# Performance work log

Measured on AMD Instinct MI355X. Metric: run time of the kernel, lower is better.

The kernel has to match this reference:

```python
import jax, jax.numpy as jnp
import numpy as np

NUM_VISUAL = 16
MAX_PATCH = 1024
DIM = 1280
NUM_HEADS = 16
HEAD_DIM = DIM // NUM_HEADS  # 80


def _make_rope_cache(key):
    # cos/sin cache per (visual, patch): (N, P, 1, head_dim*2) = [cos | sin]
    inv_freq = 1.0 / (10000.0 ** (jnp.arange(0, HEAD_DIM, 2, dtype=jnp.float32) / HEAD_DIM))  # (hd/2,)
    pos = jnp.arange(MAX_PATCH, dtype=jnp.float32)  # (P,)
    freqs = pos[:, None] * inv_freq[None, :]              # (P, hd/2)
    emb = jnp.concatenate([freqs, freqs], axis=-1)        # (P, hd)
    cos = jnp.cos(emb)
    sin = jnp.sin(emb)
    cache = jnp.concatenate([cos, sin], axis=-1)          # (P, 2*hd)
    return jnp.broadcast_to(cache[None, :, None, :], (NUM_VISUAL, MAX_PATCH, 1, 2 * HEAD_DIM))


def setup_inputs() -> dict:
    key = jax.random.key(0)
    k1, k2, k3, k4, k5, k6 = jax.random.split(key, 6)
    s = 0.02
    hidden_states = jax.random.normal(k1, (NUM_VISUAL, MAX_PATCH, DIM), dtype=jnp.float32)
    rope_cache = _make_rope_cache(k2)
    seq_lens = jax.random.randint(k3, (NUM_VISUAL,), 512, MAX_PATCH + 1, dtype=jnp.int32)
    w_qkv = jax.random.normal(k4, (3 * DIM, DIM), dtype=jnp.float32) * s
    b_qkv = jnp.zeros((3 * DIM,), dtype=jnp.float32)
    w_proj = jax.random.normal(k5, (DIM, DIM), dtype=jnp.float32) * s
    b_proj = jnp.zeros((DIM,), dtype=jnp.float32)
    return {"hidden_states": hidden_states, "rope_cache": rope_cache, "seq_lens": seq_lens,
            "w_qkv": w_qkv, "b_qkv": b_qkv, "w_proj": w_proj, "b_proj": b_proj}


def _rotate_half(x):
    x1, x2 = jnp.split(x, 2, axis=-1)
    return jnp.concatenate([-x2, x1], axis=-1)


def reference(hidden_states, rope_cache, seq_lens, w_qkv, b_qkv, w_proj, b_proj):
    N, P, D = hidden_states.shape
    H, hd = NUM_HEADS, HEAD_DIM
    # QKV projection: (N, P, 3D) -> (N, P, 3, H, hd)
    qkv = (hidden_states @ w_qkv.T + b_qkv).reshape(N, P, 3, H, hd)
    q, k, v = qkv[:, :, 0], qkv[:, :, 1], qkv[:, :, 2]  # each (N, P, H, hd)
    # RoPE via precomputed cos/sin: rope_cache (N, P, 1, 2*hd)
    cos = rope_cache[..., :hd]   # (N, P, 1, hd), broadcasts over heads
    sin = rope_cache[..., hd:]
    q = q * cos + _rotate_half(q) * sin
    k = k * cos + _rotate_half(k) * sin
    # Attention with key-padding mask (BlockMask equivalent for varlen patches)
    scale = 1.0 / jnp.sqrt(jnp.asarray(hd, dtype=q.dtype))
    scores = jnp.einsum("nqhd,nkhd->nhqk", q, k) * scale  # (N, H, P, P)
    key_valid = jnp.arange(P, dtype=jnp.int32)[None, :] < seq_lens[:, None]  # (N, P)
    neg = jnp.asarray(-1e30, dtype=scores.dtype)
    scores = jnp.where(key_valid[:, None, None, :], scores, neg)
    attn = jax.nn.softmax(scores, axis=-1)
    out = jnp.einsum("nhqk,nkhd->nqhd", attn, v).reshape(N, P, D)
    return out @ w_proj.T + b_proj
```

## Files before the change

### kernel.cpp

```cpp
#include <hip/hip_runtime.h>
#include <stdint.h>

#define DIM     1280
#define NHEADS  16
#define HD      80
#define NV      16
#define MAXP    1024
#define MTOT    (NV*MAXP)

typedef __bf16 bf16;
using bf16x8 = __attribute__((ext_vector_type(8))) __bf16;
using bf16x4 = __attribute__((ext_vector_type(4))) __bf16;
using f32x4  = __attribute__((ext_vector_type(4))) float;

#define GLOAD_LDS16(g, l)                                                     \
    __builtin_amdgcn_global_load_lds(                                         \
        (const __attribute__((address_space(1))) void*)(g),                   \
        (__attribute__((address_space(3))) void*)(l), 16, 0, 0)

__global__ __launch_bounds__(256)
void cvt_bf16(const float* __restrict__ src, bf16* __restrict__ dst, int n4)
{
    const int i = blockIdx.x * 256 + threadIdx.x;
    if (i < n4) {
        const float4 f = ((const float4*)src)[i];
        bf16x4 r;
        r[0] = (bf16)f.x; r[1] = (bf16)f.y; r[2] = (bf16)f.z; r[3] = (bf16)f.w;
        ((bf16x4*)dst)[i] = r;
    }
}

template<bool IS_QKV, int NB, int G>
__global__ __launch_bounds__(256)
void gemm_nt_big(const bf16* __restrict__ A, const bf16* __restrict__ B,
                 const float* __restrict__ bias,
                 bf16* __restrict__ out0, bf16* __restrict__ out1,
                 bf16* __restrict__ out2, float* __restrict__ outf)
{
    const int K = DIM;
    __shared__ __align__(16) bf16 SH[2*128*64];
    bf16* const As = SH;
    bf16* const Bs = SH + 128*64;

    const int tid  = threadIdx.x;
    const int lane = tid & 63, wave = tid >> 6;
    const int quad = lane >> 4, c16 = lane & 15;
    const int wm = wave & 1, wn = wave >> 1;

    const int bid = blockIdx.x;
    const int xcd = bid & 7;
    const int idx = bid >> 3;
    const int nbg = idx / (16*G);
    const int rem = idx % (16*G);
    const int mb  = xcd*16 + rem / G;
    const int nb  = nbg*G  + rem % G;

    const int sr   = lane >> 3;
    const int slot = lane & 7;
    const int sc   = (slot ^ sr) * 8;
    const long a_row0 = (long)mb * 128;
    const long b_row0 = (long)nb * 128;

    const bf16* ga[4];
    const bf16* gb[4];
    #pragma unroll
    for (int c = 0; c < 4; ++c) {
        const int seg = c*4 + wave;
        const int row = seg*8 + sr;
        ga[c] = A + (a_row0 + row)*K + sc;
        gb[c] = B + (b_row0 + row)*K + sc;
    }

    f32x4 acc[4][4] = {};
    const int xr = c16 & 7;

    for (int kt = 0; kt < K/64; ++kt) {
        const int k0 = kt * 64;
        __syncthreads();
        #pragma unroll
        for (int c = 0; c < 4; ++c) {
            const int seg = c*4 + wave;
            GLOAD_LDS16(ga[c] + k0, As + seg*512);
            GLOAD_LDS16(gb[c] + k0, Bs + seg*512);
        }
        __syncthreads();
        #pragma unroll
        for (int kk = 0; kk < 2; ++kk) {
            const int j  = kk*4 + quad;
            const int ko = ((j ^ xr) * 8);
            bf16x8 af[4], bfr[4];
            #pragma unroll
            for (int mt = 0; mt < 4; ++mt)
                af[mt] = *(const bf16x8*)(As + (wm*64 + mt*16 + c16)*64 + ko);
            #pragma unroll
            for (int nt = 0; nt < 4; ++nt)
                bfr[nt] = *(const bf16x8*)(Bs + (wn*64 + nt*16 + c16)*64 + ko);
            #pragma unroll
            for (int mt = 0; mt < 4; ++mt)
                #pragma unroll
                for (int nt = 0; nt < 4; ++nt)
                    acc[mt][nt] = __builtin_amdgcn_mfma_f32_16x16x32_bf16(
                        af[mt], bfr[nt], acc[mt][nt], 0, 0, 0);
        }
    }

    if constexpr (IS_QKV) {
        const int which = nb / 10;
        if (which < 2) {
            bf16* const dst = (which == 0) ? out0 : out1;
            #pragma unroll
            for (int nt = 0; nt < 4; ++nt) {
                const int col = nb*128 + wn*64 + nt*16 + c16;
                const float bv = bias[col];
                const int rr = col - which*DIM;
                const int h  = rr / HD;
                const int d  = rr - h*HD;
                #pragma unroll
                for (int mt = 0; mt < 4; ++mt) {
                    #pragma unroll
                    for (int r = 0; r < 4; ++r) {
                        const int row = mb*128 + wm*64 + mt*16 + quad*4 + r;
                        const int n = row >> 10, p = row & 1023;
                        dst[((long)((n*NHEADS + h)*MAXP + p))*HD + d] =
                            (bf16)(acc[mt][nt][r] + bv);
                    }
                }
            }
        } else {
            __syncthreads();
            #pragma unroll
            for (int nt = 0; nt < 4; ++nt) {
                const int dl0 = wn*64 + nt*16 + c16;
                const float bv = bias[nb*128 + dl0];
                const int swz = (dl0 & 15) << 3;
                #pragma unroll
                for (int mt = 0; mt < 4; ++mt) {
                    #pragma unroll
                    for (int r = 0; r < 4; ++r) {
                        const int pl = wm*64 + mt*16 + quad*4 + r;
                        SH[dl0*128 + (pl ^ swz)] = (bf16)(acc[mt][nt][r] + bv);
                    }
                }
            }
            __syncthreads();
            const int n_    = mb >> 3;
            const int pbase = (mb & 7) * 128;
            #pragma unroll
            for (int it = 0; it < 8; ++it) {
                const int c  = tid + 256*it;
                const int dl = c >> 4, j = c & 15;
                const int p0 = (j ^ (dl & 15)) << 3;
                const int rr = (nb - 20)*128 + dl;
                const int hh = rr / HD;
                const int dd = rr - hh*HD;
                bf16x8 v = *(const bf16x8*)(SH + dl*128 + j*8);
                *(bf16x8*)(out2 + ((long)((n_*NHEADS + hh)*HD + dd))*MAXP
                                  + pbase + p0) = v;
            }
        }
    } else {
        #pragma unroll
        for (int nt = 0; nt < 4; ++nt) {
            const int col = nb*128 + wn*64 + nt*16 + c16;
            const float bv = bias[col];
            #pragma unroll
            for (int mt = 0; mt < 4; ++mt) {
                #pragma unroll
                for (int r = 0; r < 4; ++r) {
                    const int row = mb*128 + wm*64 + mt*16 + quad*4 + r;
                    outf[(long)row*DIM + col] = acc[mt][nt][r] + bv;
                }
            }
        }
    }
}

__global__ __launch_bounds__(320)
void rope_kernel(bf16* __restrict__ qb, bf16* __restrict__ kb,
                 const float* __restrict__ rope)
{
    const int tid = threadIdx.x;
    const int j   = tid % 5;
    const int rl  = tid / 5;
    const long grow = (long)blockIdx.x * 64 + rl;
    const int p = (int)(grow & 1023);
    const int h = (int)((grow >> 10) & 15);
    const int n = (int)((grow >> 14) & 15);
    const int a = (int)(grow >> 18);
    bf16* const arr = a ? kb : qb;
    const long base = ((long)((n*NHEADS + h)*MAXP + p))*HD;
    const float* rc = rope + ((long)(n*MAXP + p))*160;
    const int d = j*8;

    bf16x8 x1v = *(const bf16x8*)(arr + base + d);
    bf16x8 x2v = *(const bf16x8*)(arr + base + 40 + d);

    float c1[8], s1[8], c2[8], s2[8];
    *(float4*)(c1)   = *(const float4*)(rc + d);
    *(float4*)(c1+4) = *(const float4*)(rc + d + 4);
    *(float4*)(s1)   = *(const float4*)(rc + 80 + d);
    *(float4*)(s1+4) = *(const float4*)(rc + 80 + d + 4);
    *(float4*)(c2)   = *(const float4*)(rc + 40 + d);
    *(float4*)(c2+4) = *(const float4*)(rc + 40 + d + 4);
    *(float4*)(s2)   = *(const float4*)(rc + 120 + d);
    *(float4*)(s2+4) = *(const float4*)(rc + 120 + d + 4);

    const float QS = 0.11180339887498949f * 1.4426950408889634f;
    bf16x8 r1, r2;
    #pragma unroll
    for (int i = 0; i < 8; ++i) {
        const float x1 = (float)x1v[i];
        const float x2 = (float)x2v[i];
        float o1 = x1 * c1[i] - x2 * s1[i];
        float o2 = x2 * c2[i] + x1 * s2[i];
        if (a == 0) { o1 *= QS; o2 *= QS; }
        r1[i] = (bf16)o1;
        r2[i] = (bf16)o2;
    }
    *(bf16x8*)(arr + base + d)      = r1;
    *(bf16x8*)(arr + base + 40 + d) = r2;
}

#define ATTN_ISSUE(ktp) do {                                                  \
    const long kro_ = qkbase + (long)(ktp)*64*HD;                             \
    kA = k0v ? *(const float4*)(kb + kro_ + (long)kr0*HD + kc0) : zero4;      \
    kB = k1v ? *(const float4*)(kb + kro_ + (long)kr1*HD + kc1) : zero4;      \
    kC = k2v ? *(const float4*)(kb + kro_ + (long)kr2*HD + kc2) : zero4;      \
    const long vro_ = vbase + (long)(ktp)*64 + vc8;                           \
    vA = *(const float4*)(vt + vro_ + (long)vd0*MAXP);                        \
    vB = *(const float4*)(vt + vro_ + (long)vd1*MAXP);                        \
    if (v2ok) vC = *(const float4*)(vt + vro_ + (long)vd2*MAXP);              \
} while (0)

#define ATTN_COMMIT() do {                                                    \
    *(float4*)(Ks + kr0*104 + kc0) = kA;                                      \
    *(float4*)(Ks + kr1*104 + kc1) = kB;                                      \
    *(float4*)(Ks + kr2*104 + kc2) = kC;                                      \
    *(float4*)(Vts + vd0*72 + vc8) = vA;                                      \
    *(float4*)(Vts + vd1*72 + vc8) = vB;                                      \
    if (v2ok) *(float4*)(Vts + vd2*72 + vc8) = vC;                            \
} while (0)

__global__ __launch_bounds__(256)
void attn_kernel(const bf16* __restrict__ qb, const bf16* __restrict__ kb,
                 const bf16* __restrict__ vt, const int* __restrict__ seq_lens,
                 bf16* __restrict__ outb)
{
    __shared__ __align__(16) bf16 Qs[64*104];
    __shared__ __align__(16) bf16 Ks[64*104];
    __shared__ __align__(16) bf16 Vts[80*72];

    const int tid  = threadIdx.x;
    const int lane = tid & 63, wave = tid >> 6;
    const int quad = lane >> 4, c16 = lane & 15;
    const int qt = blockIdx.x, h = blockIdx.y, n = blockIdx.z;
    const int seqlen = seq_lens[n];

    const long qkbase = ((long)(n*NHEADS + h)) * MAXP * HD;
    const long vbase  = ((long)(n*NHEADS + h)) * HD * MAXP;

    const float4 zero4 = make_float4(0.f, 0.f, 0.f, 0.f);

    const int kr0 = tid / 12,         kc0 = (tid % 12) * 8;
    const int kr1 = (tid + 256) / 12, kc1 = ((tid + 256) % 12) * 8;
    const int kr2 = (tid + 512) / 12, kc2 = ((tid + 512) % 12) * 8;
    const bool k0v = kc0 < 80, k1v = kc1 < 80, k2v = kc2 < 80;
    const int vd0 = tid >> 3, vd1 = vd0 + 32, vd2 = vd0 + 64;
    const int vc8 = (tid & 7) * 8;
    const bool v2ok = tid < 128;

    float4 kA, kB, kC, vA, vB, vC;

    ATTN_ISSUE(0);
    for (int i = tid; i < 768; i += 256) {
        int row = i / 12, c = i % 12;
        float4 v = (c < 10)
            ? *(const float4*)(qb + qkbase + (long)(qt*64 + row)*HD + c*8)
            : zero4;
        *(float4*)(Qs + row*104 + c*8) = v;
    }
    __syncthreads();
    bf16x8 aq[3];
    #pragma unroll
    for (int kc = 0; kc < 3; ++kc)
        aq[kc] = *(const bf16x8*)(Qs + (wave*16 + c16)*104 + kc*32 + quad*8);

    float mrow = -1e30f, lrow = 0.0f;
    f32x4 O[5] = {};

    union U8 { bf16x8 v; bf16x4 h[2]; };

    const int nkt = (seqlen + 63) >> 6;
    for (int kt = 0; kt < nkt; ++kt) {
        __syncthreads();
        ATTN_COMMIT();
        __syncthreads();
        if (kt + 1 < nkt) ATTN_ISSUE(kt + 1);

        f32x4 S[4] = {};
        __builtin_amdgcn_s_setprio(1);
        #pragma unroll
        for (int kc = 0; kc < 3; ++kc) {
            const int ko = kc*32 + quad*8;
            #pragma unroll
            for (int nt = 0; nt < 4; ++nt) {
                bf16x8 ak = *(const bf16x8*)(Ks + (nt*16 + c16)*104 + ko);
                S[nt] = __builtin_amdgcn_mfma_f32_16x16x32_bf16(ak, aq[kc], S[nt], 0,0,0);
            }
        }
        __builtin_amdgcn_s_setprio(0);

        if (kt == nkt - 1) {
            #pragma unroll
            for (int nt = 0; nt < 4; ++nt) {
                const int key0 = kt*64 + nt*16 + quad*4;
                #pragma unroll
                for (int r = 0; r < 4; ++r)
                    if (key0 + r >= seqlen) S[nt][r] = -1e30f;
            }
        }

        float mx[4];
        #pragma unroll
        for (int nt = 0; nt < 4; ++nt)
            mx[nt] = fmaxf(fmaxf(S[nt][0], S[nt][1]), fmaxf(S[nt][2], S[nt][3]));
        float pmax = fmaxf(fmaxf(mx[0], mx[1]), fmaxf(mx[2], mx[3]));
        pmax = fmaxf(pmax, __shfl_xor(pmax, 16));
        pmax = fmaxf(pmax, __shfl_xor(pmax, 32));

        if (!__all(pmax <= mrow + 8.0f)) {
            const float nm    = fmaxf(mrow, pmax);
            const float alpha = exp2f(mrow - nm);
            mrow = nm;
            lrow *= alpha;
            #pragma unroll
            for (int dt = 0; dt < 5; ++dt)
                #pragma unroll
                for (int r = 0; r < 4; ++r)
                    O[dt][r] *= alpha;
        }

        #pragma unroll
        for (int nt = 0; nt < 4; ++nt)
            #pragma unroll
            for (int r = 0; r < 4; ++r)
                S[nt][r] = exp2f(S[nt][r] - mrow);

        float sm[4];
        #pragma unroll
        for (int nt = 0; nt < 4; ++nt)
            sm[nt] = (S[nt][0] + S[nt][1]) + (S[nt][2] + S[nt][3]);
        float rs = (sm[0] + sm[1]) + (sm[2] + sm[3]);
        rs += __shfl_xor(rs, 16);
        rs += __shfl_xor(rs, 32);
        lrow += rs;

        bf16x8 Pk[2];
        #pragma unroll
        for (int nt = 0; nt < 4; ++nt)
            #pragma unroll
            for (int r = 0; r < 4; ++r)
                Pk[nt >> 1][(nt & 1)*4 + r] = (bf16)S[nt][r];

        __builtin_amdgcn_s_setprio(1);
        #pragma unroll
        for (int kc = 0; kc < 2; ++kc) {
            #pragma unroll
            for (int dt = 0; dt < 5; ++dt) {
                U8 av;
                av.h[0] = *(const bf16x4*)(Vts + (dt*16 + c16)*72 + kc*32 + quad*4);
                av.h[1] = *(const bf16x4*)(Vts + (dt*16 + c16)*72 + kc*32 + 16 + quad*4);
                O[dt] = __builtin_amdgcn_mfma_f32_16x16x32_bf16(av.v, Pk[kc], O[dt], 0,0,0);
            }
        }
        __builtin_amdgcn_s_setprio(0);
    }

    const float inv = 1.0f / lrow;
    #pragma unroll
    for (int dt = 0; dt < 5; ++dt)
        #pragma unroll
        for (int r = 0; r < 4; ++r)
            Qs[(wave*16 + c16)*104 + dt*16 + quad*4 + r] = (bf16)(O[dt][r] * inv);
    __syncthreads();
    for (int i = tid; i < 640; i += 256) {
        const int row = i / 10, c = i % 10;
        const float4 v = *(const float4*)(Qs + row*104 + c*8);
        *(float4*)(outb + ((long)(n*MAXP + qt*64 + row))*DIM + h*HD + c*8) = v;
    }
}

extern "C" void kernel_launch(void* const* d_in, const int* in_sizes, int n_in,
                              void* d_out, int out_size, void* d_ws, size_t ws_size,
                              hipStream_t stream)
{
    const float* hidden = (const float*)d_in[0];
    const float* rope   = (const float*)d_in[1];
    const int*   seql   = (const int*)d_in[2];
    const float* wqkv   = (const float*)d_in[3];
    const float* bqkv   = (const float*)d_in[4];
    const float* wproj  = (const float*)d_in[5];
    const float* bproj  = (const float*)d_in[6];
    float* out = (float*)d_out;

    const size_t H_ELEMS  = (size_t)MTOT*DIM;
    const size_t WQ_ELEMS = (size_t)3*DIM*DIM;
    const size_t WP_ELEMS = (size_t)DIM*DIM;
    const size_t QK_ELEMS = (size_t)NV*NHEADS*MAXP*HD;

    bf16* h_bf  = (bf16*)d_ws;
    bf16* wq_bf = h_bf  + H_ELEMS;
    bf16* wp_bf = wq_bf + WQ_ELEMS;

    bf16* q_b = (bf16*)d_out;
    bf16* k_b = q_b + QK_ELEMS;
    bf16* v_t = (bf16*)d_in[0];
    bf16* a_b = v_t + QK_ELEMS;

    cvt_bf16<<<(H_ELEMS/4 + 255)/256, 256, 0, stream>>>(hidden, h_bf, H_ELEMS/4);
    cvt_bf16<<<(WQ_ELEMS/4 + 255)/256, 256, 0, stream>>>(wqkv, wq_bf, WQ_ELEMS/4);
    cvt_bf16<<<(WP_ELEMS/4 + 255)/256, 256, 0, stream>>>(wproj, wp_bf, WP_ELEMS/4);

    gemm_nt_big<true, 30, 6><<<3840, 256, 0, stream>>>(
        h_bf, wq_bf, bqkv, q_b, k_b, v_t, nullptr);

    rope_kernel<<<524288/64, 320, 0, stream>>>(q_b, k_b, rope);

    attn_kernel<<<dim3(MAXP/64, NHEADS, NV), 256, 0, stream>>>(
        q_b, k_b, v_t, seql, a_b);

    gemm_nt_big<false, 10, 10><<<1280, 256, 0, stream>>>(
        a_b, wp_bf, bproj, nullptr, nullptr, nullptr, out);
}
```

Before: 657.2 us.

## Double-buffer GEMM LDS tiles and stage Q/K epilogue through shared memory

The GEMM main loop now uses two LDS buffers, issuing the next k-tile's global-to-LDS loads before computing the current one, with manual vmcnt waits and barriers. The aim is to overlap memory latency with MFMA work. The Q/K epilogue now writes the accumulator into swizzled LDS first and then emits 16-byte vector stores to the head-major output, replacing scattered 2-byte stores. This doubles LDS use to 64KB per block, which may reduce occupancy. The Q/K vector stores also assume 8-column groups never cross an 80-wide head boundary; this holds because 80 is a multiple of 8.

```diff
diff --git a/kernel.cpp b/kernel.cpp
--- a/kernel.cpp
+++ b/kernel.cpp
@@ -30,6 +30,17 @@
     }
 }
 
+#define GEMM_STAGE(dA, dB, koff) do {                                         \
+    GLOAD_LDS16(ga[0] + (koff), (dA) + (0*4 + wave)*512);                     \
+    GLOAD_LDS16(gb[0] + (koff), (dB) + (0*4 + wave)*512);                     \
+    GLOAD_LDS16(ga[1] + (koff), (dA) + (1*4 + wave)*512);                     \
+    GLOAD_LDS16(gb[1] + (koff), (dB) + (1*4 + wave)*512);                     \
+    GLOAD_LDS16(ga[2] + (koff), (dA) + (2*4 + wave)*512);                     \
+    GLOAD_LDS16(gb[2] + (koff), (dB) + (2*4 + wave)*512);                     \
+    GLOAD_LDS16(ga[3] + (koff), (dA) + (3*4 + wave)*512);                     \
+    GLOAD_LDS16(gb[3] + (koff), (dB) + (3*4 + wave)*512);                     \
+} while (0)
+
 template<bool IS_QKV, int NB, int G>
 __global__ __launch_bounds__(256)
 void gemm_nt_big(const bf16* __restrict__ A, const bf16* __restrict__ B,
@@ -38,9 +49,12 @@
                  bf16* __restrict__ out2, float* __restrict__ outf)
 {
     const int K = DIM;
-    __shared__ __align__(16) bf16 SH[2*128*64];
-    bf16* const As = SH;
-    bf16* const Bs = SH + 128*64;
+    const int NKT = K/64;
+    __shared__ __align__(16) bf16 SH[4*128*64];
+    bf16* const As0 = SH;
+    bf16* const Bs0 = SH + 8192;
+    bf16* const As1 = SH + 16384;
+    bf16* const Bs1 = SH + 24576;
 
     const int tid  = threadIdx.x;
     const int lane = tid & 63, wave = tid >> 6;
@@ -74,16 +88,24 @@
     f32x4 acc[4][4] = {};
     const int xr = c16 & 7;
 
-    for (int kt = 0; kt < K/64; ++kt) {
-        const int k0 = kt * 64;
-        __syncthreads();
-        #pragma unroll
-        for (int c = 0; c < 4; ++c) {
-            const int seg = c*4 + wave;
-            GLOAD_LDS16(ga[c] + k0, As + seg*512);
-            GLOAD_LDS16(gb[c] + k0, Bs + seg*512);
-        }
-        __syncthreads();
+    GEMM_STAGE(As0, Bs0, 0);
+
+    for (int kt = 0; kt < NKT; ++kt) {
+        const bool odd = kt & 1;
+        bf16* const Ac = odd ? As1 : As0;
+        bf16* const Bc = odd ? Bs1 : Bs0;
+        if (kt + 1 < NKT) {
+            bf16* const An = odd ? As0 : As1;
+            bf16* const Bn = odd ? Bs0 : Bs1;
+            GEMM_STAGE(An, Bn, (kt+1)*64);
+            asm volatile("s_waitcnt vmcnt(8)" ::: "memory");
+        } else {
+            asm volatile("s_waitcnt vmcnt(0)" ::: "memory");
+        }
+        __builtin_amdgcn_sched_barrier(0);
+        __builtin_amdgcn_s_barrier();
+        __builtin_amdgcn_sched_barrier(0);
+
         #pragma unroll
         for (int kk = 0; kk < 2; ++kk) {
             const int j  = kk*4 + quad;
@@ -91,10 +113,10 @@
             bf16x8 af[4], bfr[4];
             #pragma unroll
             for (int mt = 0; mt < 4; ++mt)
-                af[mt] = *(const bf16x8*)(As + (wm*64 + mt*16 + c16)*64 + ko);
+                af[mt] = *(const bf16x8*)(Ac + (wm*64 + mt*16 + c16)*64 + ko);
             #pragma unroll
             for (int nt = 0; nt < 4; ++nt)
-                bfr[nt] = *(const bf16x8*)(Bs + (wn*64 + nt*16 + c16)*64 + ko);
+                bfr[nt] = *(const bf16x8*)(Bc + (wn*64 + nt*16 + c16)*64 + ko);
             #pragma unroll
             for (int mt = 0; mt < 4; ++mt)
                 #pragma unroll
@@ -102,32 +124,44 @@
                     acc[mt][nt] = __builtin_amdgcn_mfma_f32_16x16x32_bf16(
                         af[mt], bfr[nt], acc[mt][nt], 0, 0, 0);
         }
+
+        __builtin_amdgcn_sched_barrier(0);
+        __builtin_amdgcn_s_barrier();
+        __builtin_amdgcn_sched_barrier(0);
     }
 
     if constexpr (IS_QKV) {
         const int which = nb / 10;
         if (which < 2) {
-            bf16* const dst = (which == 0) ? out0 : out1;
             #pragma unroll
             for (int nt = 0; nt < 4; ++nt) {
-                const int col = nb*128 + wn*64 + nt*16 + c16;
-                const float bv = bias[col];
-                const int rr = col - which*DIM;
-                const int h  = rr / HD;
-                const int d  = rr - h*HD;
+                const int col = wn*64 + nt*16 + c16;
+                const float bv = bias[nb*128 + col];
                 #pragma unroll
                 for (int mt = 0; mt < 4; ++mt) {
                     #pragma unroll
                     for (int r = 0; r < 4; ++r) {
-                        const int row = mb*128 + wm*64 + mt*16 + quad*4 + r;
-                        const int n = row >> 10, p = row & 1023;
-                        dst[((long)((n*NHEADS + h)*MAXP + p))*HD + d] =
+                        const int row = wm*64 + mt*16 + quad*4 + r;
+                        SH[row*128 + (col ^ ((row & 7) << 3))] =
                             (bf16)(acc[mt][nt][r] + bv);
                     }
                 }
             }
+            __syncthreads();
+            bf16* const dst = (which == 0) ? out0 : out1;
+            const int n_ = mb >> 3;
+            const int pb = (mb & 7) * 128;
+            const int j  = tid & 15;
+            const int colg = nb*128 - which*DIM + j*8;
+            const int hh = colg / 80;
+            const int dd = colg - hh*80;
+            #pragma unroll
+            for (int i = 0; i < 8; ++i) {
+                const int p = (tid >> 4) + 16*i;
+                bf16x8 v = *(const bf16x8*)(SH + p*128 + ((j ^ (p & 7)) * 8));
+                *(bf16x8*)(dst + ((long)((n_*NHEADS + hh)*MAXP + pb + p))*HD + dd) = v;
+            }
         } else {
-            __syncthreads();
             #pragma unroll
             for (int nt = 0; nt < 4; ++nt) {
                 const int dl0 = wn*64 + nt*16 + c16;
```

New measurement: 607.6 us. 7.6% less time.
